# Kernel tuning notes

Measured on AMD Instinct MI355X. Metric: run time of the kernel, lower is better.

Reference implementation:

```python
import jax, jax.numpy as jnp
import numpy as np

EMBED, HEADS, LEVELS, POINTS = 256, 8, 1, 4


def setup_inputs():
    key = jax.random.key(0)
    ks = jax.random.split(key, 8)
    B, NQ = 8, 8192
    Hh, Ww = 128, 128
    E, Hn, L, P = EMBED, HEADS, LEVELS, POINTS
    s = 1.0 / np.sqrt(E)
    return dict(
        query=jax.random.normal(ks[0], (B, NQ, E), jnp.float32),
        value=jax.random.normal(ks[1], (B, Hh * Ww, E), jnp.float32),
        ref_2d=jax.random.uniform(ks[2], (B, NQ, L, 2), dtype=jnp.float32),
        spatial_shapes=jnp.array([[Hh, Ww]], dtype=jnp.int32),
        W_off=jax.random.normal(ks[3], (E, Hn * L * P * 2), jnp.float32) * 0.01,
        b_off=jax.random.normal(ks[4], (Hn * L * P * 2,), jnp.float32) * 0.5,
        W_attn=jax.random.normal(ks[5], (E, Hn * L * P), jnp.float32) * s,
        b_attn=jnp.zeros((Hn * L * P,), jnp.float32),
        W_val=jax.random.normal(ks[6], (E, E), jnp.float32) * s,
        b_val=jnp.zeros((E,), jnp.float32),
        W_out=jax.random.normal(ks[7], (E, E), jnp.float32) * s,
        b_out=jnp.zeros((E,), jnp.float32),
    )


def _bilinear_sample(v, loc, Hl, Wl):
    # v: (B, Hn, Hl*Wl, dh); loc: (B, Hn, NQ, P, 2) normalized [0,1] (x, y)
    B, Hn, NQ, P, _ = loc.shape
    dh = v.shape[-1]
    # torch grid_sample(align_corners=False) pixel coords: p = loc * size - 0.5
    x = loc[..., 0] * Wl - 0.5
    y = loc[..., 1] * Hl - 0.5
    x0 = jnp.floor(x); y0 = jnp.floor(y)
    x1 = x0 + 1.0; y1 = y0 + 1.0
    wx1 = x - x0; wx0 = 1.0 - wx1
    wy1 = y - y0; wy0 = 1.0 - wy1

    def corner(xc, yc, w):
        valid = (xc >= 0) & (xc < Wl) & (yc >= 0) & (yc < Hl)  # zeros padding
        xi = jnp.clip(xc, 0, Wl - 1).astype(jnp.int32)
        yi = jnp.clip(yc, 0, Hl - 1).astype(jnp.int32)
        idx = (yi * Wl + xi).reshape(B, Hn, NQ * P, 1)
        vals = jnp.take_along_axis(v, idx, axis=2).reshape(B, Hn, NQ, P, dh)
        return vals * (w * valid.astype(v.dtype))[..., None]

    return (corner(x0, y0, wx0 * wy0) + corner(x1, y0, wx1 * wy0)
            + corner(x0, y1, wx0 * wy1) + corner(x1, y1, wx1 * wy1))


def _forward(query, value, ref_2d, W_off, b_off, W_attn, b_attn, W_val, b_val, W_out, b_out, shapes):
    B, NQ, E = query.shape
    Hn, L, P = HEADS, LEVELS, POINTS
    dh = E // Hn
    NV = value.shape[1]
    identity = query
    v = (value @ W_val + b_val).reshape(B, NV, Hn, dh)
    off = (query @ W_off + b_off).reshape(B, NQ, Hn, L, P, 2)
    attn = jax.nn.softmax((query @ W_attn + b_attn).reshape(B, NQ, Hn, L * P), axis=-1)
    attn = attn.reshape(B, NQ, Hn, L, P)
    # offset_normalizer = (W, H) per level
    norm = jnp.asarray(shapes[:, ::-1].copy(), dtype=query.dtype)
    loc = ref_2d[:, :, None, :, None, :] + off / norm[None, None, None, :, None, :]
    loc = jnp.transpose(loc, (0, 2, 1, 3, 4, 5))   # (B, Hn, NQ, L, P, 2)
    attn_t = jnp.transpose(attn, (0, 2, 1, 3, 4))  # (B, Hn, NQ, L, P)
    v_t = jnp.transpose(v, (0, 2, 1, 3))           # (B, Hn, NV, dh)
    starts = np.concatenate([[0], np.cumsum(shapes[:, 0] * shapes[:, 1])]).astype(np.int64)
    out = jnp.zeros((B, Hn, NQ, dh), query.dtype)
    for l in range(L):  # static small loop over feature levels
        Hl, Wl = int(shapes[l, 0]), int(shapes[l, 1])
        v_l = v_t[:, :, int(starts[l]):int(starts[l + 1]), :]
        samp = _bilinear_sample(v_l, loc[:, :, :, l], Hl, Wl)  # (B,Hn,NQ,P,dh)
        out = out + jnp.sum(samp * attn_t[:, :, :, l, :, None], axis=3)
    out = jnp.transpose(out, (0, 2, 1, 3)).reshape(B, NQ, E)
    # dropout is identity at eval time
    return out @ W_out + b_out + identity


def reference(query, value, ref_2d, spatial_shapes, W_off, b_off, W_attn, b_attn, W_val, b_val, W_out, b_out):
    shapes = np.asarray(jax.device_get(spatial_shapes))  # static level shapes
    return _forward(query, value, ref_2d, W_off, b_off, W_attn, b_attn, W_val, b_val, W_out, b_out, shapes)
```

## Files before the change

kernel.cpp:

```cpp
#include <hip/hip_runtime.h>

typedef short s16x8 __attribute__((ext_vector_type(8)));
typedef float f32x4 __attribute__((ext_vector_type(4)));

#define HN 8
#define PP 4
#define DH 32
#define NQc 8192
#define NVc 16384
#define EE 256
#define HWc 128

__device__ __forceinline__ unsigned short f2bf(float x) {
  unsigned u = __float_as_uint(x);
  u += 0x7FFF + ((u >> 16) & 1);
  return (unsigned short)(u >> 16);
}
__device__ __forceinline__ float bf2f(unsigned short h) {
  return __uint_as_float(((unsigned)h) << 16);
}

__global__ __launch_bounds__(256) void wprep(
    const float* __restrict__ Wval, const float* __restrict__ Wout,
    const float* __restrict__ Woff, const float* __restrict__ Wattn,
    const float* __restrict__ boff, const float* __restrict__ battn,
    unsigned short* __restrict__ wvt, unsigned short* __restrict__ wot,
    unsigned short* __restrict__ wct, float* __restrict__ bcat) {
  int g = blockIdx.x * 256 + threadIdx.x;
  if (g < 65536) {
    int n = g >> 8, k = g & 255;
    wvt[n * 256 + k] = f2bf(Wval[k * 256 + n]);
  } else if (g < 131072) {
    int g2 = g - 65536;
    int n = g2 >> 8, k = g2 & 255;
    wot[n * 256 + k] = f2bf(Wout[k * 256 + n]);
  } else if (g < 163840) {
    int g2 = g - 131072;
    int n = g2 >> 8, k = g2 & 255;
    float v = 0.f;
    if (n < 64) v = Woff[k * 64 + n];
    else if (n < 96) v = Wattn[k * 32 + (n - 64)];
    wct[n * 256 + k] = f2bf(v);
  } else if (g < 163968) {
    int c = g - 163840;
    bcat[c] = (c < 64) ? boff[c] : ((c < 96) ? battn[c - 64] : 0.f);
  }
}

#define MODE_VAL 0
#define MODE_PLAIN 1
#define MODE_OUT 2

template <int MODE>
struct SmemBytes { static constexpr int v = 40960; };
template <> struct SmemBytes<MODE_PLAIN> { static constexpr int v = 51200; };

template <int MODE, bool ABF16>
__global__ __launch_bounds__(256) void mfma_gemm(
    const void* __restrict__ Ain, const unsigned short* __restrict__ Wt,
    const float* __restrict__ bias, const float* __restrict__ resid,
    const float* __restrict__ ref2d, unsigned int* __restrict__ meta,
    void* __restrict__ outp) {
  __shared__ __align__(16) char smem[SmemBytes<MODE>::v];
  unsigned short* As0 = (unsigned short*)smem;
  unsigned short* Ws0 = As0 + 128 * 40;
  unsigned short* As1 = Ws0 + 128 * 40;
  unsigned short* Ws1 = As1 + 128 * 40;
  const int t = threadIdx.x;
  const int lane = t & 63, wave = t >> 6;
  const int lane15 = lane & 15, quad = lane >> 4;
  const int wr = wave >> 1, wc = wave & 1;
  const int bm = blockIdx.x * 128, bn = blockIdx.y * 128;

  f32x4 acc[4][4];
#pragma unroll
  for (int i = 0; i < 4; ++i)
#pragma unroll
    for (int j = 0; j < 4; ++j)
#pragma unroll
      for (int r = 0; r < 4; ++r) acc[i][j][r] = 0.f;

  const int ar = t >> 3, ac = (t & 7) * 4;
  const int wr2 = t >> 1, wcp = (t & 1) * 2;

  float4 av[4];
  uint4 ab0, ab1, wv0, wv1;

#define LOAD_TILE(K0)                                                          \
  do {                                                                         \
    if (!ABF16) {                                                              \
      const float* Af = (const float*)Ain;                                     \
      _Pragma("unroll") for (int i = 0; i < 4; ++i)                            \
          av[i] = *(const float4*)(Af + (size_t)(bm + ar + i * 32) * 256 +     \
                                   (K0) + ac);                                 \
    } else {                                                                   \
      const unsigned short* Ab = (const unsigned short*)Ain;                   \
      ab0 = *(const uint4*)(Ab + (size_t)(bm + wr2) * 256 + (K0) + wcp * 8);   \
      ab1 = *(const uint4*)(Ab + (size_t)(bm + wr2) * 256 + (K0) + wcp * 8 + 8); \
    }                                                                          \
    wv0 = *(const uint4*)(Wt + (size_t)(bn + wr2) * 256 + (K0) + wcp * 8);     \
    wv1 = *(const uint4*)(Wt + (size_t)(bn + wr2) * 256 + (K0) + wcp * 8 + 8); \
  } while (0)

#define STAGE(AsD, WsD)                                                        \
  do {                                                                         \
    if (!ABF16) {                                                              \
      _Pragma("unroll") for (int i = 0; i < 4; ++i) {                          \
        ushort4 c;                                                             \
        c.x = f2bf(av[i].x); c.y = f2bf(av[i].y);                              \
        c.z = f2bf(av[i].z); c.w = f2bf(av[i].w);                              \
        *(ushort4*)&(AsD)[(ar + i * 32) * 40 + ac] = c;                        \
      }                                                                        \
    } else {                                                                   \
      *(uint4*)&(AsD)[wr2 * 40 + wcp * 8] = ab0;                               \
      *(uint4*)&(AsD)[wr2 * 40 + wcp * 8 + 8] = ab1;                           \
    }                                                                          \
    *(uint4*)&(WsD)[wr2 * 40 + wcp * 8] = wv0;                                 \
    *(uint4*)&(WsD)[wr2 * 40 + wcp * 8 + 8] = wv1;                             \
  } while (0)

  LOAD_TILE(0);
  STAGE(As0, Ws0);
  __syncthreads();

#pragma unroll
  for (int kk = 0; kk < 8; ++kk) {
    unsigned short* Ar = (kk & 1) ? As1 : As0;
    unsigned short* Wr = (kk & 1) ? Ws1 : Ws0;
    if (kk < 7) LOAD_TILE((kk + 1) * 32);
    s16x8 af[4], bfr[4];
#pragma unroll
    for (int tm = 0; tm < 4; ++tm)
      af[tm] = *(const s16x8*)&Ar[(wr * 64 + tm * 16 + lane15) * 40 + quad * 8];
#pragma unroll
    for (int tn = 0; tn < 4; ++tn)
      bfr[tn] = *(const s16x8*)&Wr[(wc * 64 + tn * 16 + lane15) * 40 + quad * 8];
#pragma unroll
    for (int tm = 0; tm < 4; ++tm)
#pragma unroll
      for (int tn = 0; tn < 4; ++tn)
        acc[tm][tn] = __builtin_amdgcn_mfma_f32_16x16x32_bf16(bfr[tn], af[tm], acc[tm][tn], 0, 0, 0);
    if (kk < 7) {
      unsigned short* Aw = (kk & 1) ? As0 : As1;
      unsigned short* Ww = (kk & 1) ? Ws0 : Ws1;
      STAGE(Aw, Ww);
      __syncthreads();
    }
  }
#undef LOAD_TILE
#undef STAGE

  if (MODE == MODE_VAL) {
    unsigned short* outs = (unsigned short*)outp;
    const size_t b = (size_t)(bm >> 14);
    const int n0 = bm & (NVc - 1);
#pragma unroll
    for (int tn = 0; tn < 4; ++tn) {
      const int ch0 = bn + wc * 64 + tn * 16 + quad * 4;
      const float4 b4 = *(const float4*)&bias[ch0];
      const int h = ch0 >> 5, dh0 = ch0 & 31;
#pragma unroll
      for (int tm = 0; tm < 4; ++tm) {
        const int n = n0 + wr * 64 + tm * 16 + lane15;
        ushort4 o;
        o.x = f2bf(acc[tm][tn][0] + b4.x);
        o.y = f2bf(acc[tm][tn][1] + b4.y);
        o.z = f2bf(acc[tm][tn][2] + b4.z);
        o.w = f2bf(acc[tm][tn][3] + b4.w);
        *(ushort4*)(outs + ((b * HN + h) * NVc + n) * DH + dh0) = o;
      }
    }
  } else if (MODE == MODE_PLAIN) {
    float* Cf = (float*)smem;
    __syncthreads();
#pragma unroll
    for (int tn = 0; tn < 4; ++tn) {
      const int col0 = wc * 64 + tn * 16 + quad * 4;
      if (col0 < 96) {
        const float4 b4 = *(const float4*)&bias[col0];
#pragma unroll
        for (int tm = 0; tm < 4; ++tm) {
          const int m = wr * 64 + tm * 16 + lane15;
          float4 v;
          v.x = acc[tm][tn][0] + b4.x;
          v.y = acc[tm][tn][1] + b4.y;
          v.z = acc[tm][tn][2] + b4.z;
          v.w = acc[tm][tn][3] + b4.w;
          *(float4*)&Cf[m * 100 + col0] = v;
        }
      }
    }
    __syncthreads();
#pragma unroll
    for (int i = 0; i < 4; ++i) {
      const int task = i * 256 + t;
      const int h = task & 7, rowl = task >> 3;
      const int bq = bm + rowl;
      const float* row = Cf + rowl * 100;
      const float rx = ref2d[(size_t)bq * 2 + 0];
      const float ry = ref2d[(size_t)bq * 2 + 1];
      const float l0 = row[64 + h * 4 + 0], l1 = row[64 + h * 4 + 1];
      const float l2 = row[64 + h * 4 + 2], l3 = row[64 + h * 4 + 3];
      const float mx = fmaxf(fmaxf(l0, l1), fmaxf(l2, l3));
      float e0 = __expf(l0 - mx), e1 = __expf(l1 - mx), e2 = __expf(l2 - mx), e3 = __expf(l3 - mx);
      const float inv = 1.0f / (e0 + e1 + e2 + e3);
      float ee[4] = {e0, e1, e2, e3};
      unsigned int* m = meta + ((size_t)bq * 8 + h) * 20;
      uint4 pk;
      float4 wts[4];
#pragma unroll
      for (int p = 0; p < PP; ++p) {
        const float a = ee[p] * inv;
        const float ox = row[h * 8 + p * 2 + 0];
        const float oy = row[h * 8 + p * 2 + 1];
        const float x = (rx + ox * (1.0f / HWc)) * (float)HWc - 0.5f;
        const float y = (ry + oy * (1.0f / HWc)) * (float)HWc - 0.5f;
        const float x0f = floorf(x), y0f = floorf(y);
        const int x0 = (int)x0f, y0 = (int)y0f;
        const float wx1 = x - x0f, wx0 = 1.f - wx1;
        const float wy1 = y - y0f, wy0 = 1.f - wy1;
        const bool vx0 = (unsigned)x0 < (unsigned)HWc, vx1 = (unsigned)(x0 + 1) < (unsigned)HWc;
        const bool vy0 = (unsigned)y0 < (unsigned)HWc, vy1 = (unsigned)(y0 + 1) < (unsigned)HWc;
        const int xi0 = min(max(x0, 0), HWc - 1), xi1 = min(max(x0 + 1, 0), HWc - 1);
        const int yi0 = min(max(y0, 0), HWc - 1), yi1 = min(max(y0 + 1, 0), HWc - 1);
        const unsigned pv = (unsigned)xi0 | ((unsigned)yi0 << 8) | ((unsigned)xi1 << 16) | ((unsigned)yi1 << 24);
        if (p == 0) pk.x = pv; else if (p == 1) pk.y = pv; else if (p == 2) pk.z = pv; else pk.w = pv;
        float4 w;
        w.x = (vx0 && vy0) ? a * wx0 * wy0 : 0.f;
        w.y = (vx1 && vy0) ? a * wx1 * wy0 : 0.f;
        w.z = (vx0 && vy1) ? a * wx0 * wy1 : 0.f;
        w.w = (vx1 && vy1) ? a * wx1 * wy1 : 0.f;
        wts[p] = w;
      }
      *(uint4*)m = pk;
#pragma unroll
      for (int p = 0; p < PP; ++p) *(float4*)&m[4 + p * 4] = wts[p];
    }
  } else {
    float* Cf = (float*)smem;
    float* outf = (float*)outp;
#pragma unroll
    for (int pass = 0; pass < 2; ++pass) {
      __syncthreads();
      if (wr == pass) {
#pragma unroll
        for (int tn = 0; tn < 4; ++tn) {
          const int col0 = wc * 64 + tn * 16 + quad * 4;
          const float4 b4 = *(const float4*)&bias[bn + col0];
#pragma unroll
          for (int tm = 0; tm < 4; ++tm) {
            const int rowl = tm * 16 + lane15;
            float4 v;
            v.x = acc[tm][tn][0] + b4.x;
            v.y = acc[tm][tn][1] + b4.y;
            v.z = acc[tm][tn][2] + b4.z;
            v.w = acc[tm][tn][3] + b4.w;
            *(float4*)&Cf[rowl * 132 + col0] = v;
          }
        }
      }
      __syncthreads();
#pragma unroll
      for (int i = 0; i < 8; ++i) {
        const int id = i * 256 + t;
        const int n = id >> 5, c = id & 31;
        const size_t row = (size_t)bm + pass * 64 + n;
        float4 v = *(const float4*)&Cf[n * 132 + c * 4];
        float4 rs = *(const float4*)(resid + row * 256 + bn + c * 4);
        v.x += rs.x; v.y += rs.y; v.z += rs.z; v.w += rs.w;
        *(float4*)(outf + row * 256 + bn + c * 4) = v;
      }
    }
  }
}

__global__ __launch_bounds__(256) void sample_kernel(
    const unsigned short* __restrict__ vbuf,
    const unsigned int* __restrict__ meta,
    unsigned short* __restrict__ outs) {
  const int t = threadIdx.x;
  const int d4 = (t & 7) << 2;
  const int ql = t >> 3;
  const int sl = blockIdx.x >> 8;
  const int qc = blockIdx.x & 255;
  const int b = sl >> 3;
  const int h = sl & 7;
  const int q = qc * 32 + ql;
  const size_t bq = (size_t)b * NQc + q;
  const unsigned int* m = meta + ((size_t)bq * 8 + h) * 20;
  const uint4 pk = *(const uint4*)m;
  const unsigned short* vb = vbuf + (size_t)sl * (NVc * DH) + d4;

  float4 acc = {0.f, 0.f, 0.f, 0.f};
#pragma unroll
  for (int p = 0; p < PP; ++p) {
    const unsigned P = (p == 0) ? pk.x : (p == 1) ? pk.y : (p == 2) ? pk.z : pk.w;
    const float4 w = *(const float4*)(m + 4 + p * 4);
    const int x0 = P & 255, y0 = (P >> 8) & 255, x1 = (P >> 16) & 255, y1 = P >> 24;
    const int r0 = y0 << 12, r1 = y1 << 12;
    const ushort4 v00 = *(const ushort4*)(vb + r0 + (x0 << 5));
    const ushort4 v10 = *(const ushort4*)(vb + r0 + (x1 << 5));
    const ushort4 v01 = *(const ushort4*)(vb + r1 + (x0 << 5));
    const ushort4 v11 = *(const ushort4*)(vb + r1 + (x1 << 5));
    acc.x += w.x * bf2f(v00.x); acc.y += w.x * bf2f(v00.y);
    acc.z += w.x * bf2f(v00.z); acc.w += w.x * bf2f(v00.w);
    acc.x += w.y * bf2f(v10.x); acc.y += w.y * bf2f(v10.y);
    acc.z += w.y * bf2f(v10.z); acc.w += w.y * bf2f(v10.w);
    acc.x += w.z * bf2f(v01.x); acc.y += w.z * bf2f(v01.y);
    acc.z += w.z * bf2f(v01.z); acc.w += w.z * bf2f(v01.w);
    acc.x += w.w * bf2f(v11.x); acc.y += w.w * bf2f(v11.y);
    acc.z += w.w * bf2f(v11.z); acc.w += w.w * bf2f(v11.w);
  }
  ushort4 o;
  o.x = f2bf(acc.x); o.y = f2bf(acc.y); o.z = f2bf(acc.z); o.w = f2bf(acc.w);
  *(ushort4*)(outs + bq * EE + h * DH + d4) = o;
}

extern "C" void kernel_launch(void* const* d_in, const int* in_sizes, int n_in,
                              void* d_out, int out_size, void* d_ws, size_t ws_size,
                              hipStream_t stream) {
  const float* query = (const float*)d_in[0];
  const float* value = (const float*)d_in[1];
  const float* ref2d = (const float*)d_in[2];
  const float* Woff  = (const float*)d_in[4];
  const float* boff  = (const float*)d_in[5];
  const float* Wattn = (const float*)d_in[6];
  const float* battn = (const float*)d_in[7];
  const float* Wval  = (const float*)d_in[8];
  const float* bval  = (const float*)d_in[9];
  const float* Wout  = (const float*)d_in[10];
  const float* bout  = (const float*)d_in[11];
  float* out = (float*)d_out;

  unsigned short* vbuf = (unsigned short*)d_ws;
  unsigned int* meta   = (unsigned int*)(vbuf + 33554432);
  unsigned short* sbuf = (unsigned short*)(meta + 10485760);
  unsigned short* wvt  = sbuf + 16777216;
  unsigned short* wot  = wvt + 65536;
  unsigned short* wct  = wot + 65536;
  float* bcat          = (float*)(wct + 32768);

  wprep<<<641, 256, 0, stream>>>(Wval, Wout, Woff, Wattn, boff, battn, wvt, wot, wct, bcat);

  mfma_gemm<MODE_VAL, false><<<dim3(1024, 2), 256, 0, stream>>>(
      (const void*)value, wvt, bval, nullptr, nullptr, nullptr, (void*)vbuf);

  mfma_gemm<MODE_PLAIN, false><<<dim3(512, 1), 256, 0, stream>>>(
      (const void*)query, wct, bcat, nullptr, ref2d, meta, nullptr);

  sample_kernel<<<16384, 256, 0, stream>>>(vbuf, meta, sbuf);

  mfma_gemm<MODE_OUT, true><<<dim3(512, 2), 256, 0, stream>>>(
      (const void*)sbuf, wot, bout, query, nullptr, nullptr, (void*)out);
}
```

Before: 426.0 us.

## Stream GEMM tiles via global_load_lds with XOR swizzle and in-LDS bf16 conversion

Replaces the register-staged global loads and LDS stores in the MFMA GEMM with direct global-to-LDS loads (global_load_lds, 16 bytes per lane). The LDS layout uses an XOR-swizzled slot index instead of padding. For fp32 A inputs, the raw fp32 tile now sits in LDS and is converted to bf16 with v_cvt_pk_bf16_f32 at fragment-read time. The goal is to cut VGPR staging and instruction overhead and to overlap copies with MFMA. The cost is a larger LDS footprint for fp32 A and reliance on an implicit wait at the barrier before tiles are consumed.

```diff
diff --git a/kernel.cpp b/kernel.cpp
--- a/kernel.cpp
+++ b/kernel.cpp
@@ -18,6 +18,16 @@
 }
 __device__ __forceinline__ float bf2f(unsigned short h) {
   return __uint_as_float(((unsigned)h) << 16);
+}
+__device__ __forceinline__ unsigned cvt2(float lo, float hi) {
+  unsigned r;
+  asm("v_cvt_pk_bf16_f32 %0, %1, %2" : "=v"(r) : "v"(lo), "v"(hi));
+  return r;
+}
+__device__ __forceinline__ void gld16(const void* g, void* l) {
+  __builtin_amdgcn_global_load_lds(
+      (const __attribute__((address_space(1))) void*)g,
+      (__attribute__((address_space(3))) void*)l, 16, 0, 0);
 }
 
 __global__ __launch_bounds__(256) void wprep(
@@ -52,8 +62,9 @@
 #define MODE_OUT 2
 
 template <int MODE>
-struct SmemBytes { static constexpr int v = 40960; };
+struct SmemBytes { static constexpr int v = 49152; };
 template <> struct SmemBytes<MODE_PLAIN> { static constexpr int v = 51200; };
+template <> struct SmemBytes<MODE_OUT>   { static constexpr int v = 33792; };
 
 template <int MODE, bool ABF16>
 __global__ __launch_bounds__(256) void mfma_gemm(
@@ -62,10 +73,12 @@
     const float* __restrict__ ref2d, unsigned int* __restrict__ meta,
     void* __restrict__ outp) {
   __shared__ __align__(16) char smem[SmemBytes<MODE>::v];
-  unsigned short* As0 = (unsigned short*)smem;
-  unsigned short* Ws0 = As0 + 128 * 40;
-  unsigned short* As1 = Ws0 + 128 * 40;
-  unsigned short* Ws1 = As1 + 128 * 40;
+  constexpr int ATILE = ABF16 ? 8192 : 16384;
+  char* A0 = smem;
+  char* A1 = smem + ATILE;
+  unsigned short* W0 = (unsigned short*)(smem + 2 * ATILE);
+  unsigned short* W1 = W0 + 4096;
+
   const int t = threadIdx.x;
   const int lane = t & 63, wave = t >> 6;
   const int lane15 = lane & 15, quad = lane >> 4;
@@ -80,75 +93,83 @@
 #pragma unroll
       for (int r = 0; r < 4; ++r) acc[i][j][r] = 0.f;
 
-  const int ar = t >> 3, ac = (t & 7) * 4;
-  const int wr2 = t >> 1, wcp = (t & 1) * 2;
-
-  float4 av[4];
-  uint4 ab0, ab1, wv0, wv1;
-
-#define LOAD_TILE(K0)                                                          \
+  const unsigned short* Wtb = Wt + (size_t)bn * 256;
+#define ISSUE_W(K0, WD)                                                        \
+  do {                                                                         \
+    _Pragma("unroll") for (int i = 0; i < 2; ++i) {                            \
+      const int ii = wave * 2 + i;                                             \
+      const int row = ii * 16 + (lane >> 2);                                   \
+      const int slot = (lane & 3) ^ ((lane >> 2) & 3);                         \
+      gld16(Wtb + (size_t)row * 256 + (K0) + slot * 8, (WD) + ii * 512);       \
+    }                                                                          \
+  } while (0)
+#define ISSUE_A(K0, AD)                                                        \
   do {                                                                         \
     if (!ABF16) {                                                              \
-      const float* Af = (const float*)Ain;                                     \
-      _Pragma("unroll") for (int i = 0; i < 4; ++i)                            \
-          av[i] = *(const float4*)(Af + (size_t)(bm + ar + i * 32) * 256 +     \
-                                   (K0) + ac);                                 \
-    } else {                                                                   \
-      const unsigned short* Ab = (const unsigned short*)Ain;                   \
-      ab0 = *(const uint4*)(Ab + (size_t)(bm + wr2) * 256 + (K0) + wcp * 8);   \
-      ab1 = *(const uint4*)(Ab + (size_t)(bm + wr2) * 256 + (K0) + wcp * 8 + 8); \
-    }                                                                          \
-    wv0 = *(const uint4*)(Wt + (size_t)(bn + wr2) * 256 + (K0) + wcp * 8);     \
-    wv1 = *(const uint4*)(Wt + (size_t)(bn + wr2) * 256 + (K0) + wcp * 8 + 8); \
-  } while (0)
-
-#define STAGE(AsD, WsD)                                                        \
-  do {                                                                         \
-    if (!ABF16) {                                                              \
+      const float* Af = (const float*)Ain + (size_t)bm * 256;                  \
       _Pragma("unroll") for (int i = 0; i < 4; ++i) {                          \
-        ushort4 c;                                                             \
-        c.x = f2bf(av[i].x); c.y = f2bf(av[i].y);                              \
-        c.z = f2bf(av[i].z); c.w = f2bf(av[i].w);                              \
-        *(ushort4*)&(AsD)[(ar + i * 32) * 40 + ac] = c;                        \
+        const int ii = wave * 4 + i;                                           \
+        const int row = ii * 8 + (lane >> 3);                                  \
+        const int slot = (lane & 7) ^ (lane >> 3);                             \
+        gld16(Af + (size_t)row * 256 + (K0) + slot * 4, (AD) + ii * 1024);     \
       }                                                                        \
     } else {                                                                   \
-      *(uint4*)&(AsD)[wr2 * 40 + wcp * 8] = ab0;                               \
-      *(uint4*)&(AsD)[wr2 * 40 + wcp * 8 + 8] = ab1;                           \
+      const unsigned short* Ab = (const unsigned short*)Ain + (size_t)bm * 256;\
+      _Pragma("unroll") for (int i = 0; i < 2; ++i) {                          \
+        const int ii = wave * 2 + i;                                           \
+        const int row = ii * 16 + (lane >> 2);                                 \
+        const int slot = (lane & 3) ^ ((lane >> 2) & 3);                       \
+        gld16(Ab + (size_t)row * 256 + (K0) + slot * 8, (AD) + ii * 1024);     \
+      }                                                                        \
     }                                                                          \
-    *(uint4*)&(WsD)[wr2 * 40 + wcp * 8] = wv0;                                 \
-    *(uint4*)&(WsD)[wr2 * 40 + wcp * 8 + 8] = wv1;                             \
   } while (0)
 
-  LOAD_TILE(0);
-  STAGE(As0, Ws0);
-  __syncthreads();
+  ISSUE_A(0, A0);
+  ISSUE_W(0, W0);
 
 #pragma unroll
   for (int kk = 0; kk < 8; ++kk) {
-    unsigned short* Ar = (kk & 1) ? As1 : As0;
-    unsigned short* Wr = (kk & 1) ? Ws1 : Ws0;
-    if (kk < 7) LOAD_TILE((kk + 1) * 32);
+    __syncthreads();
+    if (kk < 7) {
+      if (kk & 1) { ISSUE_A((kk + 1) * 32, A0); ISSUE_W((kk + 1) * 32, W0); }
+      else        { ISSUE_A((kk + 1) * 32, A1); ISSUE_W((kk + 1) * 32, W1); }
+    }
+    const char* Ar = (kk & 1) ? A1 : A0;
+    const unsigned short* Wr = (kk & 1) ? W1 : W0;
+
     s16x8 af[4], bfr[4];
 #pragma unroll
-    for (int tm = 0; tm < 4; ++tm)
-      af[tm] = *(const s16x8*)&Ar[(wr * 64 + tm * 16 + lane15) * 40 + quad * 8];
-#pragma unroll
-    for (int tn = 0; tn < 4; ++tn)
-      bfr[tn] = *(const s16x8*)&Wr[(wc * 64 + tn * 16 + lane15) * 40 + quad * 8];
+    for (int tm = 0; tm < 4; ++tm) {
+      const int row = wr * 64 + tm * 16 + lane15;
+      if (!ABF16) {
+        const float* Arf = (const float*)Ar;
+        const int r7 = lane15 & 7;
+        const f32x4 x0 = *(const f32x4*)&Arf[row * 32 + (((quad * 2)     ^ r7) * 4)];
+        const f32x4 x1 = *(const f32x4*)&Arf[row * 32 + (((quad * 2 + 1) ^ r7) * 4)];
+        union { unsigned u[4]; s16x8 v; } tu;
+        tu.u[0] = cvt2(x0[0], x0[1]); tu.u[1] = cvt2(x0[2], x0[3]);
+        tu.u[2] = cvt2(x1[0], x1[1]); tu.u[3] = cvt2(x1[2], x1[3]);
+        af[tm] = tu.v;
+      } else {
+        const unsigned short* Arb = (const unsigned short*)Ar;
+        const int r3 = lane15 & 3;
+        af[tm] = *(const s16x8*)&Arb[row * 32 + ((quad ^ r3) * 8)];
+      }
+    }
+#pragma unroll
+    for (int tn = 0; tn < 4; ++tn) {
+      const int row = wc * 64 + tn * 16 + lane15;
+      const int r3 = lane15 & 3;
+      bfr[tn] = *(const s16x8*)&Wr[row * 32 + ((quad ^ r3) * 8)];
+    }
 #pragma unroll
     for (int tm = 0; tm < 4; ++tm)
 #pragma unroll
       for (int tn = 0; tn < 4; ++tn)
         acc[tm][tn] = __builtin_amdgcn_mfma_f32_16x16x32_bf16(bfr[tn], af[tm], acc[tm][tn], 0, 0, 0);
-    if (kk < 7) {
-      unsigned short* Aw = (kk & 1) ? As0 : As1;
-      unsigned short* Ww = (kk & 1) ? Ws0 : Ws1;
-      STAGE(Aw, Ww);
-      __syncthreads();
-    }
   }
-#undef LOAD_TILE
-#undef STAGE
+#undef ISSUE_A
+#undef ISSUE_W
 
   if (MODE == MODE_VAL) {
     unsigned short* outs = (unsigned short*)outp;
```

Measured after the change: 422.6 us. Within noise of the previous version (-0.8%).
